# Kernel optimization log

Measured on AMD Instinct MI355X. Metric: run time of the kernel, lower is better.

## Reference

```python
import jax, jax.numpy as jnp
import numpy as np

N_PED = 768
T_OBS = 8
T_PRED = 12
C_IN = 2
C_OUT = 5
HID = 16
CG_IN = (C_IN + 2) * T_OBS  # (C+2)*T channels after pairwise-diff reshape
TH = 1.0
TAU = 0.1
BN_EPS = 1e-5


def _conv1x1(x, w, b):
    # x: [B, Cin, H, W], w: [Cout, Cin], b: [Cout]
    return jnp.einsum('bcij,oc->boij', x, w) + b[None, :, None, None]


def _find_group_indices(dist):
    # Faithful serial union-find-style relabeling from GroupGenerator.find_group_indices.
    # Edges are strict-lower-triangular entries with dist <= TH, processed in row-major order.
    N = dist.shape[0]
    adj = jnp.tril(dist <= TH, k=-1)

    def body(k, labels):
        r = k // N
        c = k % N
        new = jnp.where(labels == labels[r], c, labels)
        return jnp.where(adj[r, c], new, labels)

    labels = jax.lax.fori_loop(0, N * N, body, jnp.arange(N))
    # remap unique labels (sorted ascending) to 0..G-1, like torch.unique + arange map
    present = jnp.zeros((N,), jnp.int32).at[labels].set(1)
    rank = jnp.cumsum(present) - 1
    return rank[labels]


def setup_inputs() -> dict:
    key = jax.random.key(0)
    ks = jax.random.split(key, 8)

    def rn(k, shape, scale=0.1):
        return jax.random.normal(k, shape, jnp.float32) * scale

    return {
        'v_abs': jax.random.normal(ks[0], (1, C_IN, T_OBS, N_PED), jnp.float32),
        'v_rel': jax.random.normal(ks[1], (1, C_IN, T_OBS, N_PED), jnp.float32),
        'vel_w': rn(ks[2], (2, C_IN)),
        'vel_b': jnp.zeros((2,), jnp.float32),
        'g1_w': rn(ks[3], (HID, CG_IN)),
        'g1_b': jnp.zeros((HID,), jnp.float32),
        'bn_gamma': jnp.ones((HID,), jnp.float32),
        'bn_beta': jnp.zeros((HID,), jnp.float32),
        'g2_w': rn(ks[4], (1, HID)),
        'g2_b': jnp.zeros((1,), jnp.float32),
        'base_wt': rn(ks[5], (T_OBS, T_PRED)),
        'base_wc': rn(ks[6], (C_IN, C_OUT)),
    }


def reference(v_abs, v_rel, vel_w, vel_b, g1_w, g1_b, bn_gamma, bn_beta, g2_w, g2_b, base_wt, base_wc):
    inv_std = 1.0 / np.sqrt(1.0 + BN_EPS)  # eval-mode BN with running (mean=0, var=1)

    # velocity extractor (1x1 conv)
    velocity = _conv1x1(v_rel, vel_w, vel_b)                    # [1,2,T,N]
    v_comb = jnp.concatenate([v_abs, velocity], axis=1)         # [1,4,T,N]

    # pairwise differences -> learned distance matrix (velocity_aware path)
    diff = v_comb[..., :, None] - v_comb[..., None, :]          # [1,4,T,N,N]
    temp = diff.reshape(1, CG_IN, N_PED, N_PED)                 # [1,32,N,N]
    h = jax.nn.relu(_conv1x1(temp, g1_w, g1_b))
    h = (h * inv_std) * bn_gamma[None, :, None, None] + bn_beta[None, :, None, None]
    d = jnp.exp(_conv1x1(h, g2_w, g2_b))                        # [1,1,N,N]
    dist = 0.5 * (d + jnp.swapaxes(d, -1, -2))                  # symmetrize
    dist_mean = dist[0].mean(axis=0)                            # [N,N]

    indices = _find_group_indices(jax.lax.stop_gradient(dist_mean))  # [N] int group ids

    # soft group assignment with straight-through hard trick
    sig = jax.nn.sigmoid(-(dist_mean - TH) / TAU)
    sig_norm = sig / sig.sum(axis=0, keepdims=True)
    v_soft = jnp.einsum('bctn,nm->bctm', v_rel, sig_norm)
    v_grouped = jax.lax.stop_gradient(v_rel - v_soft) + v_soft  # hard=True

    # linear surrogate for the injected baseline_model (DMRGCN): time-mix + channel-mix
    def baseline(v):
        return jnp.einsum('bctn,tp,co->bopn', v, base_wt, base_wc)  # [1,C_OUT,T_PRED,N]

    # branch 1: original
    v1 = baseline(v_rel)

    # branch 2: inter-group (pool -> baseline -> unpool); groups padded to N slots
    onehot = (indices[:, None] == jnp.arange(N_PED)[None, :]).astype(v_rel.dtype)  # [N,N]
    counts = onehot.sum(axis=0)                                 # [N]
    v_pool = jnp.einsum('bctn,ng->bctg', v_grouped, onehot) / jnp.maximum(counts, 1.0)
    v2 = baseline(v_pool)[..., indices]                         # unpool via gather

    # branch 3: intra-group (grouped features through baseline)
    v3 = baseline(v_grouped)

    # GroupIntegrator mix_type='mean'
    return (v1 + v2 + v3) / 3.0
```

## Files before the change

### kernel.cpp

```cpp
#include <hip/hip_runtime.h>
#include <math.h>

#define N_PED 768
#define NW 12


__global__ __launch_bounds__(256) void kb(
    const float* __restrict__ va, const float* __restrict__ vr,
    const float* __restrict__ velw, const float* __restrict__ velb,
    const float* __restrict__ g1w, const float* __restrict__ g1b,
    const float* __restrict__ gam, const float* __restrict__ bet,
    const float* __restrict__ g2w, const float* __restrict__ g2b,
    unsigned short* __restrict__ adjT16, int* __restrict__ rowmaxT) {
  int bid = blockIdx.x;
  int tile = bid >> 2, chunk = bid & 3;
  int I = tile / NW, J = tile % NW;
  int tid = threadIdx.x;
  if (I < J) {
    if (tid < 64) adjT16[(J * 64 + tid) * 48 + I * 4 + chunk] = 0;
    if (tid < 16) rowmaxT[J * N_PED + I * 64 + chunk * 16 + tid] = -1;
    return;
  }
  __shared__ double Acol[16][64];
  __shared__ double Arow[16][16];
  __shared__ unsigned long long roww[16];

  {
    int job = tid >> 1, half = tid & 1;
    bool isrow = (job >= 64);
    bool active = (job < 80) && !(isrow && I == J);
    if (active) {
      int node = isrow ? (I * 64 + chunk * 16 + (job - 64)) : (J * 64 + job);
      double F[32];
#pragma unroll
      for (int cc = 0; cc < 2; ++cc)
#pragma unroll
        for (int t = 0; t < 8; ++t)
          F[cc * 8 + t] = (double)va[(cc * 8 + t) * N_PED + node];
#pragma unroll
      for (int o = 0; o < 2; ++o)
#pragma unroll
        for (int t = 0; t < 8; ++t)
          F[(2 + o) * 8 + t] = (double)velb[o]
              + (double)velw[o * 2 + 0] * (double)vr[(0 + t) * N_PED + node]
              + (double)velw[o * 2 + 1] * (double)vr[(8 + t) * N_PED + node];
      for (int o = half * 8; o < half * 8 + 8; ++o) {
        double s = 0.0;
#pragma unroll
        for (int k = 0; k < 32; ++k) s += (double)g1w[o * 32 + k] * F[k];
        if (isrow) Arow[o][job - 64] = s;
        else Acol[o][job] = s;
      }
    }
  }
  __syncthreads();

  double w2[16], b1[16];
  const double inv_std = 1.0 / sqrt(1.0 + 1e-5);
#pragma unroll
  for (int o = 0; o < 16; ++o) {
    w2[o] = (double)g2w[o] * inv_std * (double)gam[o];
    b1[o] = (double)g1b[o];
  }
  double c0 = (double)g2b[0];
#pragma unroll
  for (int o = 0; o < 16; ++o) c0 += (double)g2w[o] * (double)bet[o];

  int w = tid >> 6, lane = tid & 63;
  int c = J * 64 + lane;
  double Ac[16];
#pragma unroll
  for (int o = 0; o < 16; ++o) Ac[o] = Acol[o][lane];

  for (int q = 0; q < 4; ++q) {
    int rr = w * 4 + q;
    int r = I * 64 + chunk * 16 + rr;
    double x1 = 0.0, x2 = 0.0;
#pragma unroll
    for (int o = 0; o < 16; ++o) {
      double Av = (I == J) ? Acol[o][chunk * 16 + rr] : Arow[o][rr];
      double s = Av - Ac[o];
      x1 += w2[o] * fmax(s + b1[o], 0.0);
      x2 += w2[o] * fmax(b1[o] - s, 0.0);
    }
    double dist = 0.5 * (exp(x1 + c0) + exp(x2 + c0));
    bool bit = (c < r) && (dist <= 1.0);
    unsigned long long word = __ballot(bit ? 1 : 0);
    if (lane == 0) {
      roww[rr] = word;
      rowmaxT[J * N_PED + r] =
          word ? (J * 64 + 63 - __clzll((long long)word)) : -1;
    }
  }
  __syncthreads();

  if (tid < 64) {
    unsigned m = 0;
#pragma unroll
    for (int rr = 0; rr < 16; ++rr)
      m |= (unsigned)((roww[rr] >> tid) & 1ull) << rr;
    adjT16[(J * 64 + tid) * 48 + I * 4 + chunk] = (unsigned short)m;
  }
}

__global__ __launch_bounds__(768) void k3s(
    const unsigned long long* __restrict__ adjT,
    const int* __restrict__ rowmaxT, int* __restrict__ out_idx) {
  __shared__ int nxtA[N_PED], nxtB[N_PED];
  __shared__ int valL[N_PED], labL[N_PED], rankL[N_PED];
  const int n = threadIdx.x;

  int cm = -1;
#pragma unroll
  for (int j = 0; j < NW; ++j) {
    int t = rowmaxT[j * N_PED + n];
    cm = t > cm ? t : cm;
  }
  int v0 = (cm >= 0) ? cm : n;
  valL[n] = v0;

  int succ = n;
  {
    int j = n >> 6, rl = n & 63;
    unsigned long long w0 = (adjT[v0 * NW + j] >> rl) >> 1;
    if (w0) {
      succ = n + __ffsll(w0);
    } else {
      for (++j; j < NW; ++j) {
        unsigned long long ww = adjT[v0 * NW + j];
        if (ww) { succ = j * 64 + __ffsll(ww) - 1; break; }
      }
    }
  }
  nxtA[n] = succ;
  __syncthreads();

  int* src = nxtA;
  int* dst = nxtB;
#pragma unroll
  for (int it = 0; it < 10; ++it) {
    dst[n] = src[src[n]];
    __syncthreads();
    int* t = src; src = dst; dst = t;
  }
  labL[n] = valL[src[n]];
  __syncthreads();

  nxtA[n] = 0;
  __syncthreads();
  nxtA[labL[n]] = 1;
  __syncthreads();
  if (n < 64) {
    int f[NW], s = 0;
#pragma unroll
    for (int q = 0; q < NW; ++q) { f[q] = nxtA[n * NW + q]; s += f[q]; }
    int inc = s;
    for (int d = 1; d < 64; d <<= 1) {
      int t = __shfl_up(inc, d);
      if (n >= d) inc += t;
    }
    int run = inc - s;
#pragma unroll
    for (int q = 0; q < NW; ++q) { run += f[q]; rankL[n * NW + q] = run - 1; }
  }
  __syncthreads();
  out_idx[n] = rankL[labL[n]];
}

__global__ __launch_bounds__(256) void k4_pool(
    const float* __restrict__ vrel, const int* __restrict__ idx,
    float* __restrict__ pool) {
  int wv = blockIdx.x * 4 + (threadIdx.x >> 6);
  int lane = threadIdx.x & 63;
  int ct = wv / N_PED;
  int g = wv % N_PED;
  float s = 0.f;
  int cnt = 0;
#pragma unroll
  for (int k = 0; k < NW; ++k) {
    int n = k * 64 + lane;
    int id = idx[n];
    float v = vrel[ct * N_PED + n];
    bool m = (id == g);
    s += m ? v : 0.f;
    cnt += m ? 1 : 0;
  }
#pragma unroll
  for (int d = 1; d < 64; d <<= 1) {
    s += __shfl_xor(s, d);
    cnt += __shfl_xor(cnt, d);
  }
  if (lane == 0) pool[ct * N_PED + g] = s / fmaxf((float)cnt, 1.0f);
}

__global__ __launch_bounds__(256) void k5_final(
    const float* __restrict__ vrel, const float* __restrict__ pool,
    const int* __restrict__ idx, const float* __restrict__ wt,
    const float* __restrict__ wc, float* __restrict__ out) {
  int i = blockIdx.x * 256 + threadIdx.x;
  if (i >= 5 * 12 * N_PED) return;
  int n = i % N_PED;
  int t_ = i / N_PED;
  int p = t_ % 12;
  int o = t_ / 12;
  int g = idx[n];
  float v1 = 0.f, v2 = 0.f;
#pragma unroll
  for (int c = 0; c < 2; ++c) {
    float u1 = 0.f, u2 = 0.f;
#pragma unroll
    for (int t = 0; t < 8; ++t) {
      float wtv = wt[t * 12 + p];
      u1 += wtv * vrel[(c * 8 + t) * N_PED + n];
      u2 += wtv * pool[(c * 8 + t) * N_PED + g];
    }
    float wcv = wc[c * 5 + o];
    v1 += wcv * u1;
    v2 += wcv * u2;
  }
  out[i] = (v1 + v2 + v1) / 3.0f;
}

extern "C" void kernel_launch(void* const* d_in, const int* in_sizes, int n_in,
                              void* d_out, int out_size, void* d_ws, size_t ws_size,
                              hipStream_t stream) {
  const float* va   = (const float*)d_in[0];
  const float* vr   = (const float*)d_in[1];
  const float* velw = (const float*)d_in[2];
  const float* velb = (const float*)d_in[3];
  const float* g1w  = (const float*)d_in[4];
  const float* g1b  = (const float*)d_in[5];
  const float* gam  = (const float*)d_in[6];
  const float* bet  = (const float*)d_in[7];
  const float* g2w  = (const float*)d_in[8];
  const float* g2b  = (const float*)d_in[9];
  const float* wt   = (const float*)d_in[10];
  const float* wc   = (const float*)d_in[11];
  float* out = (float*)d_out;

  char* ws = (char*)d_ws;
  unsigned short* adjT16 = (unsigned short*)(ws + 0);
  unsigned long long* adjT = (unsigned long long*)(ws + 0);
  int* rowmaxT = (int*)(ws + 73728);
  int* idx = (int*)(ws + 110592);
  float* pool = (float*)(ws + 113664);

  kb<<<576, 256, 0, stream>>>(va, vr, velw, velb, g1w, g1b, gam, bet, g2w, g2b,
                              adjT16, rowmaxT);
  k3s<<<1, 768, 0, stream>>>(adjT, rowmaxT, idx);
  k4_pool<<<3072, 256, 0, stream>>>(vr, idx, pool);
  k5_final<<<180, 256, 0, stream>>>(vr, pool, idx, wt, wc, out);
}
```

Measured before the change: 30.42 us.

## Fuse group pooling and final baseline mix into one per-node kernel

Merges the pooling kernel and the final output kernel into a single kernel. Each wavefront handles one pedestrian and computes that pedestrian's group pool over all 16 channel-time rows in registers. It then writes all 60 outputs for that pedestrian directly, with no pool buffer in global memory. This removes one launch and the global round trip for the pool. In exchange, the pool is recomputed redundantly for every member of a group, and output writes are now strided across N.

```diff
diff --git a/kernel.cpp b/kernel.cpp
--- a/kernel.cpp
+++ b/kernel.cpp
@@ -167,58 +167,58 @@
   out_idx[n] = rankL[labL[n]];
 }
 
-__global__ __launch_bounds__(256) void k4_pool(
+__global__ __launch_bounds__(256) void k45(
     const float* __restrict__ vrel, const int* __restrict__ idx,
-    float* __restrict__ pool) {
-  int wv = blockIdx.x * 4 + (threadIdx.x >> 6);
+    const float* __restrict__ wt, const float* __restrict__ wc,
+    float* __restrict__ out) {
+  int n = blockIdx.x * 4 + (threadIdx.x >> 6);
   int lane = threadIdx.x & 63;
-  int ct = wv / N_PED;
-  int g = wv % N_PED;
-  float s = 0.f;
+  int g = idx[n];
+
+  float s[16];
+#pragma unroll
+  for (int ct = 0; ct < 16; ++ct) s[ct] = 0.f;
   int cnt = 0;
 #pragma unroll
   for (int k = 0; k < NW; ++k) {
-    int n = k * 64 + lane;
-    int id = idx[n];
-    float v = vrel[ct * N_PED + n];
-    bool m = (id == g);
-    s += m ? v : 0.f;
-    cnt += m ? 1 : 0;
+    int m = k * 64 + lane;
+    bool mem = (idx[m] == g);
+    cnt += mem ? 1 : 0;
+#pragma unroll
+    for (int ct = 0; ct < 16; ++ct) {
+      float v = vrel[ct * N_PED + m];
+      s[ct] += mem ? v : 0.f;
+    }
   }
 #pragma unroll
   for (int d = 1; d < 64; d <<= 1) {
-    s += __shfl_xor(s, d);
     cnt += __shfl_xor(cnt, d);
-  }
-  if (lane == 0) pool[ct * N_PED + g] = s / fmaxf((float)cnt, 1.0f);
-}
-
-__global__ __launch_bounds__(256) void k5_final(
-    const float* __restrict__ vrel, const float* __restrict__ pool,
-    const int* __restrict__ idx, const float* __restrict__ wt,
-    const float* __restrict__ wc, float* __restrict__ out) {
-  int i = blockIdx.x * 256 + threadIdx.x;
-  if (i >= 5 * 12 * N_PED) return;
-  int n = i % N_PED;
-  int t_ = i / N_PED;
-  int p = t_ % 12;
-  int o = t_ / 12;
-  int g = idx[n];
-  float v1 = 0.f, v2 = 0.f;
-#pragma unroll
-  for (int c = 0; c < 2; ++c) {
-    float u1 = 0.f, u2 = 0.f;
-#pragma unroll
-    for (int t = 0; t < 8; ++t) {
-      float wtv = wt[t * 12 + p];
-      u1 += wtv * vrel[(c * 8 + t) * N_PED + n];
-      u2 += wtv * pool[(c * 8 + t) * N_PED + g];
-    }
-    float wcv = wc[c * 5 + o];
-    v1 += wcv * u1;
-    v2 += wcv * u2;
-  }
-  out[i] = (v1 + v2 + v1) / 3.0f;
+#pragma unroll
+    for (int ct = 0; ct < 16; ++ct) s[ct] += __shfl_xor(s[ct], d);
+  }
+  float cmax = fmaxf((float)cnt, 1.0f);
+  float pool[16];
+#pragma unroll
+  for (int ct = 0; ct < 16; ++ct) pool[ct] = s[ct] / cmax;
+
+  if (lane < 60) {
+    int o = lane / 12, p = lane % 12;
+    float v1 = 0.f, v2 = 0.f;
+#pragma unroll
+    for (int c = 0; c < 2; ++c) {
+      float u1 = 0.f, u2 = 0.f;
+#pragma unroll
+      for (int t = 0; t < 8; ++t) {
+        float wtv = wt[t * 12 + p];
+        u1 += wtv * vrel[(c * 8 + t) * N_PED + n];
+        u2 += wtv * pool[c * 8 + t];
+      }
+      float wcv = wc[c * 5 + o];
+      v1 += wcv * u1;
+      v2 += wcv * u2;
+    }
+    out[(o * 12 + p) * N_PED + n] = (v1 + v2 + v1) / 3.0f;
+  }
 }
 
 extern "C" void kernel_launch(void* const* d_in, const int* in_sizes, int n_in,
@@ -243,11 +243,9 @@
   unsigned long long* adjT = (unsigned long long*)(ws + 0);
   int* rowmaxT = (int*)(ws + 73728);
   int* idx = (int*)(ws + 110592);
-  float* pool = (float*)(ws + 113664);
 
   kb<<<576, 256, 0, stream>>>(va, vr, velw, velb, g1w, g1b, gam, bet, g2w, g2b,
                               adjT16, rowmaxT);
   k3s<<<1, 768, 0, stream>>>(adjT, rowmaxT, idx);
-  k4_pool<<<3072, 256, 0, stream>>>(vr, idx, pool);
-  k5_final<<<180, 256, 0, stream>>>(vr, pool, idx, wt, wc, out);
-}
+  k45<<<192, 256, 0, stream>>>(vr, idx, wt, wc, out);
+}
```

Result: slower. 45.51 us (+49.6%).
